# Performance work log

Hardware: AMD Instinct MI355X
Metric: run time of the kernel (lower is better)

## Reference

```python
import jax, jax.numpy as jnp
import numpy as np

NUM_USERS = 100000
NUM_ITEMS = 50000
EMBED_K = 64
N_LAYERS = 3
FEAT = 1024
N_EDGES = 3000000
BATCH = 16384


def setup_inputs() -> dict:
    key = jax.random.key(0)
    ks = jax.random.split(key, 10)
    Gu = 0.1 * jax.random.normal(ks[0], (NUM_USERS, EMBED_K), jnp.float32)
    Gi = 0.1 * jax.random.normal(ks[1], (NUM_ITEMS, EMBED_K), jnp.float32)
    Tu = jax.random.normal(ks[2], (NUM_USERS, EMBED_K), jnp.float32) * (6.0 / (NUM_USERS + EMBED_K)) ** 0.5
    F = jax.random.normal(ks[3], (NUM_ITEMS, FEAT), jnp.float32)
    proj_w = jax.random.normal(ks[4], (EMBED_K, FEAT), jnp.float32) * (1.0 / FEAT) ** 0.5
    proj_b = jnp.zeros((EMBED_K,), jnp.float32)
    user_edges = jax.random.randint(ks[5], (N_EDGES,), 0, NUM_USERS, jnp.int32)
    item_edges = jax.random.randint(ks[6], (N_EDGES,), 0, NUM_ITEMS, jnp.int32)
    users = jax.random.randint(ks[7], (BATCH,), 0, NUM_USERS, jnp.int32)
    items = jax.random.randint(ks[8], (BATCH,), 0, NUM_ITEMS, jnp.int32)
    return {"Gu": Gu, "Gi": Gi, "Tu": Tu, "F": F, "proj_w": proj_w, "proj_b": proj_b,
            "user_edges": user_edges, "item_edges": item_edges, "users": users, "items": items}


def _propagate(Gu, Gi, src, dst, n_layers):
    # LightGCN: n_layers of symmetric-normalized LGConv, then mean over [x0..xL]
    N = Gu.shape[0] + Gi.shape[0]
    deg = jax.ops.segment_sum(jnp.ones_like(src, jnp.float32), dst, num_segments=N)
    dinv = jnp.where(deg > 0, jax.lax.rsqrt(jnp.maximum(deg, 1.0)), 0.0)
    norm = dinv[src] * dinv[dst]  # [2E]
    x = jnp.concatenate([Gu, Gi], axis=0)  # [N, K]
    acc = x
    for _ in range(n_layers):
        x = jax.ops.segment_sum(x[src] * norm[:, None], dst, num_segments=N)
        acc = acc + x
    all_emb = acc / (n_layers + 1)
    return all_emb[:Gu.shape[0]], all_emb[Gu.shape[0]:]


def reference(Gu, Gi, Tu, F, proj_w, proj_b, user_edges, item_edges, users, items):
    nu = Gu.shape[0]
    # symmetric bipartite edges: user->item and item->user
    src = jnp.concatenate([user_edges, item_edges + nu])
    dst = jnp.concatenate([item_edges + nu, user_edges])
    gu, gi = _propagate(Gu, Gi, src, dst, N_LAYERS)
    gamma_u = gu[users]          # [B, K]
    gamma_i = gi[items]          # [B, K]
    theta_u = Tu[users]          # [B, K]
    proj = F[items] @ proj_w.T + proj_b  # [B, K]
    proj_i = proj / jnp.maximum(jnp.linalg.norm(proj, axis=1, keepdims=True), 1e-12)
    xui = jnp.sum(gamma_u * gamma_i, axis=1) + jnp.sum(theta_u * proj_i, axis=1)
    return xui
```

## Files before the change

kernel.cpp:

```cpp
#include <hip/hip_runtime.h>
#include <hip/hip_bf16.h>
#include <hip/hip_fp16.h>


#define WAVE 64
#define NBMAX 592
#define SLOTS 14336
#define ETG 1792

typedef int nt_int4 __attribute__((ext_vector_type(4)));

__device__ __forceinline__ unsigned pack2(float lo, float hi) {
    __half2 h = __floats2half2_rn(lo, hi);
    return *(unsigned*)&h;
}
__device__ __forceinline__ float2 unpack2(unsigned u) {
    __half2 h = *(__half2*)&u;
    return __half22float2(h);
}

__global__ __launch_bounds__(256) void histA_kernel(const int* __restrict__ ue,
                                                    const int* __restrict__ ie,
                                                    int* __restrict__ bh,
                                                    int E, int nu, int shift,
                                                    int NB, int NG) {
    __shared__ int lhist[NBMAX];
    int tid = threadIdx.x;
    for (int b = tid; b < NB; b += 256) lhist[b] = 0;
    __syncthreads();
    int g0 = blockIdx.x * ETG;
    int g1 = min(g0 + ETG, NG);
    for (int g = g0 + tid; g < g1; g += 256) {
        int e0 = g * 4;
        if (e0 + 3 < E) {
            nt_int4 u = __builtin_nontemporal_load((const nt_int4*)(ue + e0));
            nt_int4 v = __builtin_nontemporal_load((const nt_int4*)(ie + e0));
            atomicAdd(&lhist[(nu + v.x) >> shift], 1); atomicAdd(&lhist[u.x >> shift], 1);
            atomicAdd(&lhist[(nu + v.y) >> shift], 1); atomicAdd(&lhist[u.y >> shift], 1);
            atomicAdd(&lhist[(nu + v.z) >> shift], 1); atomicAdd(&lhist[u.z >> shift], 1);
            atomicAdd(&lhist[(nu + v.w) >> shift], 1); atomicAdd(&lhist[u.w >> shift], 1);
        } else {
            for (int e = e0; e < E; ++e) {
                atomicAdd(&lhist[(nu + ie[e]) >> shift], 1);
                atomicAdd(&lhist[ue[e] >> shift], 1);
            }
        }
    }
    __syncthreads();
    int* row = bh + (size_t)blockIdx.x * NB;
    for (int b = tid; b < NB; b += 256) row[b] = lhist[b];
}

__global__ __launch_bounds__(64) void colscan_kernel(const int* __restrict__ bh,
                                                     int* __restrict__ gb,
                                                     int* __restrict__ tot,
                                                     int NBLK, int NB) {
    int b = blockIdx.x;
    int lane = threadIdx.x;
    int carry = 0;
    for (int i0 = 0; i0 < NBLK; i0 += 64) {
        int i = i0 + lane;
        int x = (i < NBLK) ? bh[(size_t)i * NB + b] : 0;
        int v = x;
        #pragma unroll
        for (int d = 1; d < 64; d <<= 1) {
            int o = __shfl_up(v, d, 64);
            if (lane >= d) v += o;
        }
        if (i < NBLK) gb[(size_t)i * NB + b] = v - x + carry;
        carry += __shfl(v, 63, 64);
    }
    if (lane == 0) tot[b] = carry;
}

__global__ __launch_bounds__(1024) void bscan_kernel(const int* __restrict__ tot,
                                                     int* __restrict__ pbase,
                                                     int NB, int twoE) {
    __shared__ int wsum[16];
    int t = threadIdx.x;
    int v0 = (t < NB) ? tot[t] : 0;
    int lane = t & 63, w = t >> 6;
    int v = v0;
    #pragma unroll
    for (int d = 1; d < 64; d <<= 1) {
        int o = __shfl_up(v, d, 64);
        if (lane >= d) v += o;
    }
    if (lane == 63) wsum[w] = v;
    __syncthreads();
    if (t == 0) {
        int r = 0;
        #pragma unroll
        for (int k = 0; k < 16; ++k) { int s = wsum[k]; wsum[k] = r; r += s; }
        pbase[NB] = twoE;
    }
    __syncthreads();
    int excl = (v - v0) + wsum[w];
    if (t < NB) pbase[t] = excl;
}

__global__ __launch_bounds__(256) void place_kernel(const int* __restrict__ ue,
                                                    const int* __restrict__ ie,
                                                    const int* __restrict__ bh,
                                                    const int* __restrict__ gb,
                                                    const int* __restrict__ pbase,
                                                    int* __restrict__ pairs,
                                                    int E, int nu, int shift,
                                                    int NB, int NG) {
    __shared__ int slot[SLOTS];
    __shared__ int lhist[NBMAX];
    __shared__ int lcur[NBMAX];
    __shared__ int lbase[NBMAX];
    int blk = blockIdx.x, tid = threadIdx.x;
    for (int b = tid; b < NB; b += 256) {
        int c = bh[(size_t)blk * NB + b];
        lhist[b] = c;
        lbase[b] = pbase[b] + gb[(size_t)blk * NB + b];
    }
    __syncthreads();
    if (tid < 64) {
        int carry = 0;
        for (int c = 0; c < NB; c += 64) {
            int idx = c + tid;
            int x = (idx < NB) ? lhist[idx] : 0;
            int v = x;
            #pragma unroll
            for (int d = 1; d < 64; d <<= 1) {
                int o = __shfl_up(v, d, 64);
                if (tid >= d) v += o;
            }
            if (idx < NB) lcur[idx] = v - x + carry;
            carry += __shfl(v, 63, 64);
        }
    }
    __syncthreads();
    int g0 = blk * ETG;
    int g1 = min(g0 + ETG, NG);
    int mask = (1 << shift) - 1;
    for (int g = g0 + tid; g < g1; g += 256) {
        int e0 = g * 4;
        if (e0 + 3 < E) {
            nt_int4 u = __builtin_nontemporal_load((const nt_int4*)(ue + e0));
            nt_int4 v = __builtin_nontemporal_load((const nt_int4*)(ie + e0));
            int uu[4] = {u.x, u.y, u.z, u.w};
            int vv[4] = {nu + v.x, nu + v.y, nu + v.z, nu + v.w};
            #pragma unroll
            for (int t = 0; t < 4; ++t) {
                int d = vv[t], s = uu[t];
                int p = atomicAdd(&lcur[d >> shift], 1);
                slot[p] = ((d & mask) << 18) | s;
                d = uu[t]; s = vv[t];
                p = atomicAdd(&lcur[d >> shift], 1);
                slot[p] = ((d & mask) << 18) | s;
            }
        } else {
            for (int e = e0; e < E; ++e) {
                int d = nu + ie[e], s = ue[e];
                int p = atomicAdd(&lcur[d >> shift], 1);
                slot[p] = ((d & mask) << 18) | s;
                d = ue[e]; s = nu + ie[e];
                p = atomicAdd(&lcur[d >> shift], 1);
                slot[p] = ((d & mask) << 18) | s;
            }
        }
    }
    __syncthreads();
    int w = tid >> 6, lane = tid & 63;
    for (int b = w; b < NB; b += 4) {
        int c = lhist[b];
        if (!c) continue;
        int start = lcur[b] - c;
        int gb0 = lbase[b];
        for (int i = lane; i < c; i += 64)
            pairs[gb0 + i] = slot[start + i];
    }
}

__global__ __launch_bounds__(256) void build_kernel(const int* __restrict__ pairs,
                                                    const int* __restrict__ pbase,
                                                    int* __restrict__ offs,
                                                    float* __restrict__ dinv,
                                                    float* __restrict__ drt,
                                                    int* __restrict__ col,
                                                    int N, int shift, int NB, int twoE) {
    __shared__ int dcnt[512];
    __shared__ int ex[512];
    __shared__ int cur[512];
    int b = blockIdx.x, tid = threadIdx.x;
    int lo = b << shift;
    int n = min(1 << shift, N - lo);
    for (int i = tid; i < 512; i += 256) dcnt[i] = 0;
    __syncthreads();
    int pb = pbase[b];
    int cnt = pbase[b + 1] - pb;
    for (int i = tid; i < cnt; i += 256) {
        int p = pairs[pb + i];
        atomicAdd(&dcnt[p >> 18], 1);
    }
    __syncthreads();
    if (tid < 64) {
        int base = tid * 8;
        int loc[8]; int s = 0;
        #pragma unroll
        for (int k = 0; k < 8; ++k) { loc[k] = s; s += dcnt[base + k]; }
        int v = s;
        #pragma unroll
        for (int d = 1; d < 64; d <<= 1) {
            int o = __shfl_up(v, d, 64);
            if (tid >= d) v += o;
        }
        int excl = v - s;
        #pragma unroll
        for (int k = 0; k < 8; ++k) ex[base + k] = excl + loc[k];
    }
    __syncthreads();
    for (int i = tid; i < n; i += 256) {
        int c = pb + ex[i];
        cur[i] = c;
        offs[lo + i] = c;
        int d = dcnt[i];
        dinv[lo + i] = (d > 0) ? rsqrtf((float)d) : 0.0f;
        drt[lo + i]  = (d > 0) ? sqrtf((float)d)  : 0.0f;
    }
    if (b == NB - 1 && tid == 0) offs[N] = twoE;
    __syncthreads();
    for (int i = tid; i < cnt; i += 256) {
        int p = pairs[pb + i];
        int pos = atomicAdd(&cur[p >> 18], 1);
        col[pos] = p & 0x3FFFF;
    }
}

__global__ void mark_kernel(const int* __restrict__ users, const int* __restrict__ items,
                            int* __restrict__ flag, int B, int nu) {
    int b = blockIdx.x * blockDim.x + threadIdx.x;
    if (b < B) {
        flag[users[b]] = 1;
        flag[nu + items[b]] = 1;
    }
}

__global__ void compact_kernel(const int* __restrict__ flag, int* __restrict__ list,
                               int* __restrict__ cnt, int N) {
    int n = blockIdx.x * blockDim.x + threadIdx.x;
    if (n < N && flag[n]) {
        int pos = atomicAdd(cnt, 1);
        list[pos] = n;
    }
}

__global__ void init_z_kernel(const float* __restrict__ Gu, const float* __restrict__ Gi,
                              const float* __restrict__ dinv,
                              __half* __restrict__ z, int nu, int N) {
    int id = blockIdx.x * blockDim.x + threadIdx.x;
    if (id < N * 8) {
        int n = id >> 3, q = id & 7;
        const float4* src = (n < nu) ? (const float4*)Gu : (const float4*)Gi;
        int j = (n < nu) ? n : n - nu;
        float4 a0 = src[(size_t)j * 16 + q * 2];
        float4 a1 = src[(size_t)j * 16 + q * 2 + 1];
        float w = dinv[n];
        uint4 o;
        o.x = pack2(a0.x * w, a0.y * w);
        o.y = pack2(a0.z * w, a0.w * w);
        o.z = pack2(a1.x * w, a1.y * w);
        o.w = pack2(a1.z * w, a1.w * w);
        ((uint4*)z)[id] = o;
    }
}

__global__ void init_bacc_kernel(const float* __restrict__ Gu, const float* __restrict__ Gi,
                                 const int* __restrict__ users, const int* __restrict__ items,
                                 float* __restrict__ baccU, float* __restrict__ baccI, int B) {
    int id = blockIdx.x * blockDim.x + threadIdx.x;
    if (id < B * 16) {
        int b = id >> 4, q = id & 15;
        ((float4*)baccU)[id] = ((const float4*)Gu)[(size_t)users[b] * 16 + q];
        ((float4*)baccI)[id] = ((const float4*)Gi)[(size_t)items[b] * 16 + q];
    }
}

__global__ __launch_bounds__(256) void pull_kernel(const __half* __restrict__ z,
                                                   __half* __restrict__ zn,
                                                   const int* __restrict__ offs,
                                                   const int* __restrict__ col,
                                                   const float* __restrict__ dinv,
                                                   const int* __restrict__ rows,
                                                   const int* __restrict__ n_ptr, int N) {
    int wid = (blockIdx.x * blockDim.x + threadIdx.x) >> 6;
    int lane = threadIdx.x & 63;
    int nrows = rows ? *n_ptr : N;
    if (wid >= nrows) return;
    int r = rows ? rows[wid] : wid;
    int s = offs[r], e = offs[r + 1];
    int slot = lane >> 3;
    int q    = lane & 7;
    const uint4* zq = (const uint4*)z;
    float a0 = 0.f, a1 = 0.f, a2 = 0.f, a3 = 0.f;
    float a4 = 0.f, a5 = 0.f, a6 = 0.f, a7 = 0.f;
    for (int base = s; base < e; base += 64) {
        int idx = base + lane;
        int c = (idx < e) ? __builtin_nontemporal_load(col + idx) : 0;
        int n = min(64, e - base);
        int nfull = n & ~7;
        int j = 0;
        if (nfull > 0) {
            int cj = __shfl(c, slot);
            uint4 v = zq[(size_t)cj * 8 + q];
            for (j = 8; j < nfull; j += 8) {
                int cn = __shfl(c, j + slot);
                uint4 vn = zq[(size_t)cn * 8 + q];
                float2 f0 = unpack2(v.x), f1 = unpack2(v.y);
                float2 f2 = unpack2(v.z), f3 = unpack2(v.w);
                a0 += f0.x; a1 += f0.y; a2 += f1.x; a3 += f1.y;
                a4 += f2.x; a5 += f2.y; a6 += f3.x; a7 += f3.y;
                v = vn;
            }
            float2 f0 = unpack2(v.x), f1 = unpack2(v.y);
            float2 f2 = unpack2(v.z), f3 = unpack2(v.w);
            a0 += f0.x; a1 += f0.y; a2 += f1.x; a3 += f1.y;
            a4 += f2.x; a5 += f2.y; a6 += f3.x; a7 += f3.y;
            j = nfull;
        }
        if (j < n) {
            int take = n - j;
            int cj = __shfl(c, j + (slot < take ? slot : 0));
            uint4 v = zq[(size_t)cj * 8 + q];
            if (slot < take) {
                float2 f0 = unpack2(v.x), f1 = unpack2(v.y);
                float2 f2 = unpack2(v.z), f3 = unpack2(v.w);
                a0 += f0.x; a1 += f0.y; a2 += f1.x; a3 += f1.y;
                a4 += f2.x; a5 += f2.y; a6 += f3.x; a7 += f3.y;
            }
        }
    }
    #pragma unroll
    for (int d = 8; d < 64; d <<= 1) {
        a0 += __shfl_xor(a0, d, 64); a1 += __shfl_xor(a1, d, 64);
        a2 += __shfl_xor(a2, d, 64); a3 += __shfl_xor(a3, d, 64);
        a4 += __shfl_xor(a4, d, 64); a5 += __shfl_xor(a5, d, 64);
        a6 += __shfl_xor(a6, d, 64); a7 += __shfl_xor(a7, d, 64);
    }
    if (slot == 0) {
        float w = dinv[r];
        float ww = w * w;
        uint4 o;
        o.x = pack2(a0 * ww, a1 * ww);
        o.y = pack2(a2 * ww, a3 * ww);
        o.z = pack2(a4 * ww, a5 * ww);
        o.w = pack2(a6 * ww, a7 * ww);
        ((uint4*)(zn + (size_t)r * WAVE))[q] = o;
    }
}

__global__ void gather_acc_kernel(const __half* __restrict__ zn,
                                  const float* __restrict__ drt,
                                  const int* __restrict__ users, const int* __restrict__ items,
                                  float* __restrict__ baccU, float* __restrict__ baccI,
                                  int B, int nu) {
    int id = blockIdx.x * blockDim.x + threadIdx.x;
    if (id < B * 8) {
        int b = id >> 3, q = id & 7;
        int u = users[b], it = nu + items[b];
        float wu = drt[u], wi = drt[it];
        uint4 vu = ((const uint4*)(zn))[(size_t)u * 8 + q];
        uint4 vi = ((const uint4*)(zn))[(size_t)it * 8 + q];
        float2 u0 = unpack2(vu.x), u1 = unpack2(vu.y), u2 = unpack2(vu.z), u3 = unpack2(vu.w);
        float2 i0 = unpack2(vi.x), i1 = unpack2(vi.y), i2 = unpack2(vi.z), i3 = unpack2(vi.w);
        float4* bu = (float4*)baccU + (size_t)b * 16 + q * 2;
        float4* bi = (float4*)baccI + (size_t)b * 16 + q * 2;
        float4 a = bu[0];
        a.x += wu * u0.x; a.y += wu * u0.y; a.z += wu * u1.x; a.w += wu * u1.y;
        bu[0] = a;
        a = bu[1];
        a.x += wu * u2.x; a.y += wu * u2.y; a.z += wu * u3.x; a.w += wu * u3.y;
        bu[1] = a;
        a = bi[0];
        a.x += wi * i0.x; a.y += wi * i0.y; a.z += wi * i1.x; a.w += wi * i1.y;
        bi[0] = a;
        a = bi[1];
        a.x += wi * i2.x; a.y += wi * i2.y; a.z += wi * i3.x; a.w += wi * i3.y;
        bi[1] = a;
    }
}

__global__ __launch_bounds__(256) void proj_out_kernel(const float* __restrict__ baccU,
                                                       const float* __restrict__ baccI,
                                                       const float* __restrict__ Tu,
                                                       const float* __restrict__ F,
                                                       const float* __restrict__ W,
                                                       const float* __restrict__ bvec,
                                                       const int* __restrict__ users,
                                                       const int* __restrict__ items,
                                                       float* __restrict__ out,
                                                       int B, float invL) {
    const int FEATn = 1024;
    __shared__ float Ft[2][32][64];
    __shared__ float Wt[2][32][64];

    int tid = threadIdx.x;
    int tx = tid & 15;
    int ty = tid >> 4;
    int r0 = blockIdx.x * 64;

    int lr = tid >> 2;
    int lq = tid & 3;
    int frow = min(r0 + lr, B - 1);
    const float* Fp = F + (size_t)items[frow] * FEATn + lq * 4;
    const float* Wp = W + (size_t)lr * FEATn + lq * 4;

    float4 fa0 = *(const float4*)(Fp);
    float4 fa1 = *(const float4*)(Fp + 16);
    float4 wa0 = *(const float4*)(Wp);
    float4 wa1 = *(const float4*)(Wp + 16);

    float acc[4][4] = {};

    for (int kt = 0; kt < 32; ++kt) {
        int buf = kt & 1;
        #pragma unroll
        for (int i = 0; i < 4; ++i) {
            Ft[buf][lq * 4 + i][lr]      = ((const float*)&fa0)[i];
            Ft[buf][lq * 4 + 16 + i][lr] = ((const float*)&fa1)[i];
            Wt[buf][lq * 4 + i][lr]      = ((const float*)&wa0)[i];
            Wt[buf][lq * 4 + 16 + i][lr] = ((const float*)&wa1)[i];
        }
        __syncthreads();
        if (kt < 31) {
            const float* fp = Fp + (kt + 1) * 32;
            const float* wp = Wp + (kt + 1) * 32;
            fa0 = *(const float4*)(fp);
            fa1 = *(const float4*)(fp + 16);
            wa0 = *(const float4*)(wp);
            wa1 = *(const float4*)(wp + 16);
        }
        #pragma unroll 8
        for (int kk = 0; kk < 32; ++kk) {
            float4 a = *(const float4*)&Ft[buf][kk][ty * 4];
            float4 b = *(const float4*)&Wt[buf][kk][tx * 4];
            acc[0][0] = fmaf(a.x, b.x, acc[0][0]);
            acc[0][1] = fmaf(a.x, b.y, acc[0][1]);
            acc[0][2] = fmaf(a.x, b.z, acc[0][2]);
            acc[0][3] = fmaf(a.x, b.w, acc[0][3]);
            acc[1][0] = fmaf(a.y, b.x, acc[1][0]);
            acc[1][1] = fmaf(a.y, b.y, acc[1][1]);
            acc[1][2] = fmaf(a.y, b.z, acc[1][2]);
            acc[1][3] = fmaf(a.y, b.w, acc[1][3]);
            acc[2][0] = fmaf(a.z, b.x, acc[2][0]);
            acc[2][1] = fmaf(a.z, b.y, acc[2][1]);
            acc[2][2] = fmaf(a.z, b.z, acc[2][2]);
            acc[2][3] = fmaf(a.z, b.w, acc[2][3]);
            acc[3][0] = fmaf(a.w, b.x, acc[3][0]);
            acc[3][1] = fmaf(a.w, b.y, acc[3][1]);
            acc[3][2] = fmaf(a.w, b.z, acc[3][2]);
            acc[3][3] = fmaf(a.w, b.w, acc[3][3]);
        }
    }

    float4 bb = *(const float4*)(bvec + tx * 4);
    float L2 = invL * invL;
    float res[4];
    #pragma unroll
    for (int r = 0; r < 4; ++r) {
        int gr = min(r0 + ty * 4 + r, B - 1);
        float pb0 = acc[r][0] + bb.x;
        float pb1 = acc[r][1] + bb.y;
        float pb2 = acc[r][2] + bb.z;
        float pb3 = acc[r][3] + bb.w;
        float s = pb0 * pb0 + pb1 * pb1 + pb2 * pb2 + pb3 * pb3;
        #pragma unroll
        for (int d = 1; d < 16; d <<= 1) s += __shfl_xor(s, d, 64);
        float inv = 1.0f / fmaxf(sqrtf(s), 1e-12f);
        int u = users[gr];
        float4 tu = *(const float4*)(Tu + (size_t)u * WAVE + tx * 4);
        float4 gu = *(const float4*)(baccU + (size_t)gr * WAVE + tx * 4);
        float4 gi = *(const float4*)(baccI + (size_t)gr * WAVE + tx * 4);
        float dsum = L2 * (gu.x * gi.x + gu.y * gi.y + gu.z * gi.z + gu.w * gi.w)
                   + inv * (tu.x * pb0 + tu.y * pb1 + tu.z * pb2 + tu.w * pb3);
        #pragma unroll
        for (int d = 1; d < 16; d <<= 1) dsum += __shfl_xor(dsum, d, 64);
        res[r] = dsum;
    }
    if (tx == 0) {
        #pragma unroll
        for (int r = 0; r < 4; ++r) {
            int gr = r0 + ty * 4 + r;
            if (gr < B) out[gr] = res[r];
        }
    }
}

extern "C" void kernel_launch(void* const* d_in, const int* in_sizes, int n_in,
                              void* d_out, int out_size, void* d_ws, size_t ws_size,
                              hipStream_t stream) {
    const float* Gu = (const float*)d_in[0];
    const float* Gi = (const float*)d_in[1];
    const float* Tu = (const float*)d_in[2];
    const float* F  = (const float*)d_in[3];
    const float* W  = (const float*)d_in[4];
    const float* bv = (const float*)d_in[5];
    const int* ue    = (const int*)d_in[6];
    const int* ie    = (const int*)d_in[7];
    const int* users = (const int*)d_in[8];
    const int* items = (const int*)d_in[9];
    float* out = (float*)d_out;

    const int K  = 64;
    const int nu = in_sizes[0] / K;
    const int ni = in_sizes[1] / K;
    const int N  = nu + ni;
    const int E  = in_sizes[6];
    const int B  = in_sizes[8];

    int shift = 8;
    while (((N + (1 << shift) - 1) >> shift) > NBMAX) ++shift;
    const int NB = (N + (1 << shift) - 1) >> shift;

    const int NG   = (E + 3) / 4;
    const int nbS  = (NG + ETG - 1) / ETG;

    char* p = (char*)d_ws;
    auto alloc = [&](size_t bytes) -> void* {
        void* r = (void*)p;
        p += (bytes + 255) & ~(size_t)255;
        return r;
    };
    float* dinv   = (float*)alloc((size_t)N * 4);
    float* drt    = (float*)alloc((size_t)N * 4);
    int*   offs   = (int*)  alloc((size_t)(N + 1) * 4);
    int*   flags  = (int*)  alloc((size_t)N * 4);
    int*   col    = (int*)  alloc((size_t)2 * E * 4);
    __half* za    = (__half*)alloc((size_t)N * K * 2);
    __half* zb    = (__half*)alloc((size_t)N * K * 2);
    float* baccU  = (float*)alloc((size_t)B * K * 4);
    float* baccI  = (float*)alloc((size_t)B * K * 4);
    int*   list   = (int*)  alloc((size_t)2 * B * 4);
    int*   cnt    = (int*)  alloc(256);
    int*   bh     = (int*)  alloc((size_t)nbS * NB * 4);
    int*   gb     = (int*)  alloc((size_t)nbS * NB * 4);
    int*   tot    = (int*)  alloc((size_t)NBMAX * 4);
    int*   pbase  = (int*)  alloc((size_t)(NBMAX + 1) * 4);

    int* pairs = (int*)za;

    histA_kernel<<<nbS, 256, 0, stream>>>(ue, ie, bh, E, nu, shift, NB, NG);
    colscan_kernel<<<NB, 64, 0, stream>>>(bh, gb, tot, nbS, NB);
    bscan_kernel<<<1, 1024, 0, stream>>>(tot, pbase, NB, 2 * E);
    place_kernel<<<nbS, 256, 0, stream>>>(ue, ie, bh, gb, pbase, pairs,
                                          E, nu, shift, NB, NG);
    build_kernel<<<NB, 256, 0, stream>>>(pairs, pbase, offs, dinv, drt, col,
                                         N, shift, NB, 2 * E);

    hipMemsetAsync(flags, 0, (size_t)N * 4, stream);
    hipMemsetAsync(cnt, 0, 4, stream);
    mark_kernel<<<(B + 255) / 256, 256, 0, stream>>>(users, items, flags, B, nu);
    compact_kernel<<<(N + 255) / 256, 256, 0, stream>>>(flags, list, cnt, N);

    init_z_kernel<<<(N * 8 + 255) / 256, 256, 0, stream>>>(Gu, Gi, dinv, za, nu, N);
    init_bacc_kernel<<<(B * 16 + 255) / 256, 256, 0, stream>>>(Gu, Gi, users, items,
                                                               baccU, baccI, B);

    pull_kernel<<<(N + 3) / 4, 256, 0, stream>>>(za, zb, offs, col, dinv,
                                                 nullptr, nullptr, N);
    gather_acc_kernel<<<(B * 8 + 255) / 256, 256, 0, stream>>>(zb, drt, users, items,
                                                               baccU, baccI, B, nu);
    pull_kernel<<<(N + 3) / 4, 256, 0, stream>>>(zb, za, offs, col, dinv,
                                                 nullptr, nullptr, N);
    gather_acc_kernel<<<(B * 8 + 255) / 256, 256, 0, stream>>>(za, drt, users, items,
                                                               baccU, baccI, B, nu);
    pull_kernel<<<(2 * B + 3) / 4, 256, 0, stream>>>(za, zb, offs, col, dinv,
                                                     list, cnt, N);
    gather_acc_kernel<<<(B * 8 + 255) / 256, 256, 0, stream>>>(zb, drt, users, items,
                                                               baccU, baccI, B, nu);

    proj_out_kernel<<<(B + 63) / 64, 256, 0, stream>>>(baccU, baccI, Tu, F, W, bv,
                                                       users, items, out, B, 0.25f);
}
```

Before: 700.6 us.

## Drop mark/compact pass; pull last layer directly per batch row into accumulators

Removes the flag memset, mark and compact kernels that built a deduplicated list of batch rows. The last propagation layer now runs one wavefront per batch entry (2B rows, including duplicates) and adds the result straight into the fp32 accumulators, which also removes the final gather kernel. The accumulator init is fused into the first gather, eliminating a separate init_bacc pass. Duplicate users or items are now recomputed instead of shared, which adds some redundant edge reads in exchange for fewer launches and a full-N flag scan.

```diff
diff --git a/kernel.cpp b/kernel.cpp
--- a/kernel.cpp
+++ b/kernel.cpp
@@ -231,24 +231,6 @@
     }
 }
 
-__global__ void mark_kernel(const int* __restrict__ users, const int* __restrict__ items,
-                            int* __restrict__ flag, int B, int nu) {
-    int b = blockIdx.x * blockDim.x + threadIdx.x;
-    if (b < B) {
-        flag[users[b]] = 1;
-        flag[nu + items[b]] = 1;
-    }
-}
-
-__global__ void compact_kernel(const int* __restrict__ flag, int* __restrict__ list,
-                               int* __restrict__ cnt, int N) {
-    int n = blockIdx.x * blockDim.x + threadIdx.x;
-    if (n < N && flag[n]) {
-        int pos = atomicAdd(cnt, 1);
-        list[pos] = n;
-    }
-}
-
 __global__ void init_z_kernel(const float* __restrict__ Gu, const float* __restrict__ Gi,
                               const float* __restrict__ dinv,
                               __half* __restrict__ z, int nu, int N) {
@@ -269,29 +251,16 @@
     }
 }
 
-__global__ void init_bacc_kernel(const float* __restrict__ Gu, const float* __restrict__ Gi,
-                                 const int* __restrict__ users, const int* __restrict__ items,
-                                 float* __restrict__ baccU, float* __restrict__ baccI, int B) {
-    int id = blockIdx.x * blockDim.x + threadIdx.x;
-    if (id < B * 16) {
-        int b = id >> 4, q = id & 15;
-        ((float4*)baccU)[id] = ((const float4*)Gu)[(size_t)users[b] * 16 + q];
-        ((float4*)baccI)[id] = ((const float4*)Gi)[(size_t)items[b] * 16 + q];
-    }
-}
-
 __global__ __launch_bounds__(256) void pull_kernel(const __half* __restrict__ z,
                                                    __half* __restrict__ zn,
                                                    const int* __restrict__ offs,
                                                    const int* __restrict__ col,
                                                    const float* __restrict__ dinv,
-                                                   const int* __restrict__ rows,
-                                                   const int* __restrict__ n_ptr, int N) {
+                                                   int N) {
     int wid = (blockIdx.x * blockDim.x + threadIdx.x) >> 6;
     int lane = threadIdx.x & 63;
-    int nrows = rows ? *n_ptr : N;
-    if (wid >= nrows) return;
-    int r = rows ? rows[wid] : wid;
+    if (wid >= N) return;
+    int r = wid;
     int s = offs[r], e = offs[r + 1];
     int slot = lane >> 3;
     int q    = lane & 7;
@@ -350,6 +319,117 @@
         o.z = pack2(a4 * ww, a5 * ww);
         o.w = pack2(a6 * ww, a7 * ww);
         ((uint4*)(zn + (size_t)r * WAVE))[q] = o;
+    }
+}
+
+__global__ __launch_bounds__(256) void pull_batch_kernel(const __half* __restrict__ z,
+                                                         const int* __restrict__ offs,
+                                                         const int* __restrict__ col,
+                                                         const float* __restrict__ dinv,
+                                                         const int* __restrict__ users,
+                                                         const int* __restrict__ items,
+                                                         float* __restrict__ baccU,
+                                                         float* __restrict__ baccI,
+                                                         int B, int nu) {
+    int wid = (blockIdx.x * blockDim.x + threadIdx.x) >> 6;
+    int lane = threadIdx.x & 63;
+    if (wid >= 2 * B) return;
+    int r = (wid < B) ? users[wid] : nu + items[wid - B];
+    int s = offs[r], e = offs[r + 1];
+    int slot = lane >> 3;
+    int q    = lane & 7;
+    const uint4* zq = (const uint4*)z;
+    float a0 = 0.f, a1 = 0.f, a2 = 0.f, a3 = 0.f;
+    float a4 = 0.f, a5 = 0.f, a6 = 0.f, a7 = 0.f;
+    for (int base = s; base < e; base += 64) {
+        int idx = base + lane;
+        int c = (idx < e) ? __builtin_nontemporal_load(col + idx) : 0;
+        int n = min(64, e - base);
+        int nfull = n & ~7;
+        int j = 0;
+        if (nfull > 0) {
+            int cj = __shfl(c, slot);
+            uint4 v = zq[(size_t)cj * 8 + q];
+            for (j = 8; j < nfull; j += 8) {
+                int cn = __shfl(c, j + slot);
+                uint4 vn = zq[(size_t)cn * 8 + q];
+                float2 f0 = unpack2(v.x), f1 = unpack2(v.y);
+                float2 f2 = unpack2(v.z), f3 = unpack2(v.w);
+                a0 += f0.x; a1 += f0.y; a2 += f1.x; a3 += f1.y;
+                a4 += f2.x; a5 += f2.y; a6 += f3.x; a7 += f3.y;
+                v = vn;
+            }
+            float2 f0 = unpack2(v.x), f1 = unpack2(v.y);
+            float2 f2 = unpack2(v.z), f3 = unpack2(v.w);
+            a0 += f0.x; a1 += f0.y; a2 += f1.x; a3 += f1.y;
+            a4 += f2.x; a5 += f2.y; a6 += f3.x; a7 += f3.y;
+            j = nfull;
+        }
+        if (j < n) {
+            int take = n - j;
+            int cj = __shfl(c, j + (slot < take ? slot : 0));
+            uint4 v = zq[(size_t)cj * 8 + q];
+            if (slot < take) {
+                float2 f0 = unpack2(v.x), f1 = unpack2(v.y);
+                float2 f2 = unpack2(v.z), f3 = unpack2(v.w);
+                a0 += f0.x; a1 += f0.y; a2 += f1.x; a3 += f1.y;
+                a4 += f2.x; a5 += f2.y; a6 += f3.x; a7 += f3.y;
+            }
+        }
+    }
+    #pragma unroll
+    for (int d = 8; d < 64; d <<= 1) {
+        a0 += __shfl_xor(a0, d, 64); a1 += __shfl_xor(a1, d, 64);
+        a2 += __shfl_xor(a2, d, 64); a3 += __shfl_xor(a3, d, 64);
+        a4 += __shfl_xor(a4, d, 64); a5 += __shfl_xor(a5, d, 64);
+        a6 += __shfl_xor(a6, d, 64); a7 += __shfl_xor(a7, d, 64);
+    }
+    if (slot == 0) {
+        float w = dinv[r];
+        float* bp = ((wid < B) ? (baccU + (size_t)wid * WAVE)
+                               : (baccI + (size_t)(wid - B) * WAVE)) + q * 8;
+        float4 b0 = *(float4*)bp;
+        float4 b1 = *(float4*)(bp + 4);
+        b0.x += w * a0; b0.y += w * a1; b0.z += w * a2; b0.w += w * a3;
+        b1.x += w * a4; b1.y += w * a5; b1.z += w * a6; b1.w += w * a7;
+        *(float4*)bp       = b0;
+        *(float4*)(bp + 4) = b1;
+    }
+}
+
+__global__ void gather_init_kernel(const __half* __restrict__ zn,
+                                   const float* __restrict__ drt,
+                                   const float* __restrict__ Gu,
+                                   const float* __restrict__ Gi,
+                                   const int* __restrict__ users,
+                                   const int* __restrict__ items,
+                                   float* __restrict__ baccU, float* __restrict__ baccI,
+                                   int B, int nu) {
+    int id = blockIdx.x * blockDim.x + threadIdx.x;
+    if (id < B * 8) {
+        int b = id >> 3, q = id & 7;
+        int u = users[b], iti = items[b], it = nu + iti;
+        float wu = drt[u], wi = drt[it];
+        uint4 vu = ((const uint4*)(zn))[(size_t)u * 8 + q];
+        uint4 vi = ((const uint4*)(zn))[(size_t)it * 8 + q];
+        float2 u0 = unpack2(vu.x), u1 = unpack2(vu.y), u2 = unpack2(vu.z), u3 = unpack2(vu.w);
+        float2 i0 = unpack2(vi.x), i1 = unpack2(vi.y), i2 = unpack2(vi.z), i3 = unpack2(vi.w);
+        const float4* gu = (const float4*)Gu + (size_t)u * 16 + q * 2;
+        const float4* gi = (const float4*)Gi + (size_t)iti * 16 + q * 2;
+        float4* bu = (float4*)baccU + (size_t)b * 16 + q * 2;
+        float4* bi = (float4*)baccI + (size_t)b * 16 + q * 2;
+        float4 a = gu[0];
+        a.x += wu * u0.x; a.y += wu * u0.y; a.z += wu * u1.x; a.w += wu * u1.y;
+        bu[0] = a;
+        a = gu[1];
+        a.x += wu * u2.x; a.y += wu * u2.y; a.z += wu * u3.x; a.w += wu * u3.y;
+        bu[1] = a;
+        a = gi[0];
+        a.x += wi * i0.x; a.y += wi * i0.y; a.z += wi * i1.x; a.w += wi * i1.y;
+        bi[0] = a;
+        a = gi[1];
+        a.x += wi * i2.x; a.y += wi * i2.y; a.z += wi * i3.x; a.w += wi * i3.y;
+        bi[1] = a;
     }
 }
 
@@ -528,14 +608,11 @@
     float* dinv   = (float*)alloc((size_t)N * 4);
     float* drt    = (float*)alloc((size_t)N * 4);
     int*   offs   = (int*)  alloc((size_t)(N + 1) * 4);
-    int*   flags  = (int*)  alloc((size_t)N * 4);
     int*   col    = (int*)  alloc((size_t)2 * E * 4);
     __half* za    = (__half*)alloc((size_t)N * K * 2);
     __half* zb    = (__half*)alloc((size_t)N * K * 2);
     float* baccU  = (float*)alloc((size_t)B * K * 4);
     float* baccI  = (float*)alloc((size_t)B * K * 4);
-    int*   list   = (int*)  alloc((size_t)2 * B * 4);
-    int*   cnt    = (int*)  alloc(256);
     int*   bh     = (int*)  alloc((size_t)nbS * NB * 4);
     int*   gb     = (int*)  alloc((size_t)nbS * NB * 4);
     int*   tot    = (int*)  alloc((size_t)NBMAX * 4);
@@ -551,27 +628,18 @@
     build_kernel<<<NB, 256, 0, stream>>>(pairs, pbase, offs, dinv, drt, col,
                                          N, shift, NB, 2 * E);
 
-    hipMemsetAsync(flags, 0, (size_t)N * 4, stream);
-    hipMemsetAsync(cnt, 0, 4, stream);
-    mark_kernel<<<(B + 255) / 256, 256, 0, stream>>>(users, items, flags, B, nu);
-    compact_kernel<<<(N + 255) / 256, 256, 0, stream>>>(flags, list, cnt, N);
-
     init_z_kernel<<<(N * 8 + 255) / 256, 256, 0, stream>>>(Gu, Gi, dinv, za, nu, N);
-    init_bacc_kernel<<<(B * 16 + 255) / 256, 256, 0, stream>>>(Gu, Gi, users, items,
-                                                               baccU, baccI, B);
-
-    pull_kernel<<<(N + 3) / 4, 256, 0, stream>>>(za, zb, offs, col, dinv,
-                                                 nullptr, nullptr, N);
-    gather_acc_kernel<<<(B * 8 + 255) / 256, 256, 0, stream>>>(zb, drt, users, items,
-                                                               baccU, baccI, B, nu);
-    pull_kernel<<<(N + 3) / 4, 256, 0, stream>>>(zb, za, offs, col, dinv,
-                                                 nullptr, nullptr, N);
+
+    pull_kernel<<<(N + 3) / 4, 256, 0, stream>>>(za, zb, offs, col, dinv, N);
+    gather_init_kernel<<<(B * 8 + 255) / 256, 256, 0, stream>>>(zb, drt, Gu, Gi,
+                                                                users, items,
+                                                                baccU, baccI, B, nu);
+    pull_kernel<<<(N + 3) / 4, 256, 0, stream>>>(zb, za, offs, col, dinv, N);
     gather_acc_kernel<<<(B * 8 + 255) / 256, 256, 0, stream>>>(za, drt, users, items,
                                                                baccU, baccI, B, nu);
-    pull_kernel<<<(2 * B + 3) / 4, 256, 0, stream>>>(za, zb, offs, col, dinv,
-                                                     list, cnt, N);
-    gather_acc_kernel<<<(B * 8 + 255) / 256, 256, 0, stream>>>(zb, drt, users, items,
-                                                               baccU, baccI, B, nu);
+    pull_batch_kernel<<<(2 * B + 3) / 4, 256, 0, stream>>>(za, offs, col, dinv,
+                                                           users, items,
+                                                           baccU, baccI, B, nu);
 
     proj_out_kernel<<<(B + 63) / 64, 256, 0, stream>>>(baccU, baccI, Tu, F, W, bv,
                                                        users, items, out, B, 0.25f);
```

Result: faster. 661.1 us (-5.6%).
